# Performance work log

Measured on AMD Instinct MI355X. Metric: run time of the kernel, lower is better.

## Reference

```python
import jax, jax.numpy as jnp
import numpy as np

B, S, C = 2, 4096, 2048
H, D = 16, 128  # inner_dim = H*D = C
EPS = 1e-15     # processor self.eps
PAD_VAL = 1.0   # processor self.pad_val


def setup_inputs() -> dict:
    key = jax.random.key(0)
    ks = jax.random.split(key, 5)
    scale = C ** -0.5
    x = jax.random.normal(ks[0], (B, S, C), jnp.float32)
    Wq = jax.random.normal(ks[1], (C, C), jnp.float32) * scale
    Wk = jax.random.normal(ks[2], (C, C), jnp.float32) * scale
    Wv = jax.random.normal(ks[3], (C, C), jnp.float32) * scale
    Wo = jax.random.normal(ks[4], (C, C), jnp.float32) * scale
    bq = jnp.zeros((C,), jnp.float32)
    bk = jnp.zeros((C,), jnp.float32)
    bv = jnp.zeros((C,), jnp.float32)
    bo = jnp.zeros((C,), jnp.float32)
    # RoPE tables: pairs are adjacent (x.reshape(..., -1, 2)), so each freq repeats twice
    inv_freq = 1.0 / (10000.0 ** (np.arange(0, D, 2, dtype=np.float32) / D))
    freqs = np.outer(np.arange(S, dtype=np.float32), inv_freq)  # [S, D/2]
    emb = np.repeat(freqs, 2, axis=1)                            # [S, D]
    cos = jnp.asarray(np.cos(emb), jnp.float32)
    sin = jnp.asarray(np.sin(emb), jnp.float32)
    return {"x": x, "cos": cos, "sin": sin, "Wq": Wq, "bq": bq, "Wk": Wk,
            "bk": bk, "Wv": Wv, "bv": bv, "Wo": Wo, "bo": bo}


def _rope(t, cos, sin):
    # t: [B, H, S, D]; cos/sin: [S, D]; adjacent-pair rotation
    tr = t[..., 0::2]
    ti = t[..., 1::2]
    t_rot = jnp.stack([-ti, tr], axis=-1).reshape(t.shape)
    return t * cos + t_rot * sin


def reference(x, cos, sin, Wq, bq, Wk, bk, Wv, bv, Wo, bo):
    # projections -> [B, H, S, D] (matches transpose(-1,-2).reshape(B,H,D,S) split)
    q = (x @ Wq.T + bq).reshape(B, S, H, D).transpose(0, 2, 1, 3)
    k = (x @ Wk.T + bk).reshape(B, S, H, D).transpose(0, 2, 1, 3)
    v = (x @ Wv.T + bv).reshape(B, S, H, D).transpose(0, 2, 1, 3)
    # RoPE on q and k (self-attention), then ReLU feature map
    q = jax.nn.relu(_rope(q, cos, sin))
    k = jax.nn.relu(_rope(k, cos, sin))
    # pad value with ones along head_dim: torch F.pad(value,(0,0,0,1),value=1.0)
    v_pad = jnp.concatenate([v, jnp.full((B, H, S, 1), PAD_VAL, v.dtype)], axis=-1)  # [B,H,S,D+1]
    # linear attention: vk = value @ key  -> [B,H,D+1,D];  hs = vk @ query -> [B,H,D+1,S]
    vk = jnp.einsum('bhsn,bhsd->bhnd', v_pad, k)
    hs = jnp.einsum('bhnd,bhsd->bhns', vk, q)
    # eps-normalize by the padded-ones channel
    hs = hs[:, :, :-1] / (hs[:, :, -1:] + EPS)  # [B,H,D,S]
    out = hs.transpose(0, 3, 1, 2).reshape(B, S, H * D)  # view(B,H*D,S).permute(0,2,1)
    return out @ Wo.T + bo
```

## Files before the change

### kernel.cpp

```cpp
#include <hip/hip_runtime.h>


typedef unsigned short u16;
typedef __attribute__((ext_vector_type(8))) short bf16x8;
typedef __attribute__((ext_vector_type(4))) float f32x4;

__device__ __forceinline__ float bf2f(u16 u) {
    union { unsigned int i; float f; } x; x.i = ((unsigned int)u) << 16; return x.f;
}
__device__ __forceinline__ u16 f2bf(float f) {
    union { unsigned int i; float f; } x; x.f = f;
    unsigned int i = x.i;
    return (u16)((i + 0x7fffu + ((i >> 16) & 1u)) >> 16);
}
__device__ __forceinline__ uint4 pack8(const float* __restrict__ src) {
    float4 f0 = *(const float4*)(src);
    float4 f1 = *(const float4*)(src + 4);
    union { u16 u[8]; uint4 v; } P;
    P.u[0] = f2bf(f0.x); P.u[1] = f2bf(f0.y); P.u[2] = f2bf(f0.z); P.u[3] = f2bf(f0.w);
    P.u[4] = f2bf(f1.x); P.u[5] = f2bf(f1.y); P.u[6] = f2bf(f1.z); P.u[7] = f2bf(f1.w);
    return P.v;
}
__device__ __forceinline__ void gll16(void* lds, const void* g) {
    __builtin_amdgcn_global_load_lds(
        (const __attribute__((address_space(1))) unsigned int*)g,
        (__attribute__((address_space(3))) unsigned int*)lds, 16, 0, 0);
}

__global__ __launch_bounds__(256) void cast_all(
    const float* __restrict__ x,  const float* __restrict__ Wq,
    const float* __restrict__ Wk, const float* __restrict__ Wv,
    const float* __restrict__ Wo,
    u16* __restrict__ Xb, u16* __restrict__ Wqkvb, u16* __restrict__ Wob)
{
    int bid = blockIdx.x, t = threadIdx.x;
    const float* s; u16* d; size_t i;
    if (bid < 8192)       { s = x;  d = Xb;              i = (size_t)bid * 256 + t; }
    else if (bid < 10240) { s = Wq; d = Wqkvb;           i = (size_t)(bid - 8192)  * 256 + t; }
    else if (bid < 12288) { s = Wk; d = Wqkvb + 4194304; i = (size_t)(bid - 10240) * 256 + t; }
    else if (bid < 14336) { s = Wv; d = Wqkvb + 8388608; i = (size_t)(bid - 12288) * 256 + t; }
    else                  { s = Wo; d = Wob;             i = (size_t)(bid - 14336) * 256 + t; }
    *(uint4*)(d + i * 8) = pack8(s + i * 8);
}

__global__ __launch_bounds__(256) void gemm_qkv(
    const u16* __restrict__ Xb, const u16* __restrict__ Wqkvb,
    const float* __restrict__ bq, const float* __restrict__ bk, const float* __restrict__ bv,
    const float* __restrict__ cosT, const float* __restrict__ sinT,
    u16* __restrict__ Q, u16* __restrict__ K, u16* __restrict__ V)
{
    __shared__ __align__(16) u16 As[2 * 128 * 32];
    __shared__ __align__(16) u16 Bs[2 * 128 * 32];

    int t  = threadIdx.x;
    int bm = blockIdx.x;
    int bn = blockIdx.y;
    int region = bn >> 4;
    const u16*   W    = Wqkvb + (size_t)region * 4194304;
    const float* bias = (region == 0) ? bq : (region == 1 ? bk : bv);
    u16* OUT          = (region == 0) ? Q  : (region == 1 ? K  : V);

    int m0 = bm * 128;
    int n0 = (bn & 15) * 128;

    int w = t >> 6, lane = t & 63, quad = lane >> 4, l16 = lane & 15;
    int wm0 = (w >> 1) * 64, wn0 = (w & 1) * 64;
    int w32 = w * 32;
    int lr  = lane >> 2;
    int lc  = (lane & 3) * 8;

    const u16* ga = Xb + (size_t)(m0 + w32 + lr) * 2048 + lc;
    const u16* gb = W  + (size_t)(n0 + w32 + lr) * 2048 + lc;

    f32x4 acc[4][4] = {};

    for (int k0 = 0; k0 < 2048; k0 += 64) {
        __syncthreads();
#pragma unroll
        for (int p = 0; p < 2; p++) {
            gll16(As + p * 4096 + (size_t)w32 * 32,        ga + k0 + p * 32);
            gll16(As + p * 4096 + (size_t)(w32 + 16) * 32, ga + k0 + p * 32 + 16 * 2048);
            gll16(Bs + p * 4096 + (size_t)w32 * 32,        gb + k0 + p * 32);
            gll16(Bs + p * 4096 + (size_t)(w32 + 16) * 32, gb + k0 + p * 32 + 16 * 2048);
        }
        __syncthreads();

#pragma unroll
        for (int kk = 0; kk < 2; kk++) {
            bf16x8 af[4], bfr[4];
#pragma unroll
            for (int i = 0; i < 4; i++) af[i]  = *(const bf16x8*)(As + kk * 4096 + (wm0 + i * 16 + l16) * 32 + quad * 8);
#pragma unroll
            for (int j = 0; j < 4; j++) bfr[j] = *(const bf16x8*)(Bs + kk * 4096 + (wn0 + j * 16 + l16) * 32 + quad * 8);
#pragma unroll
            for (int i = 0; i < 4; i++)
#pragma unroll
                for (int j = 0; j < 4; j++)
                    acc[i][j] = __builtin_amdgcn_mfma_f32_16x16x32_bf16(af[i], bfr[j], acc[i][j], 0, 0, 0);
        }
    }

#pragma unroll
    for (int i = 0; i < 4; i++) {
#pragma unroll
        for (int j = 0; j < 4; j++) {
            int nc   = n0 + wn0 + j * 16 + l16;
            int h    = nc >> 7, dpos = nc & 127;
            float bia = bias[nc];
#pragma unroll
            for (int r = 0; r < 4; r++) {
                int mr = m0 + wm0 + i * 16 + quad * 4 + r;
                int b  = mr >> 12, s = mr & 4095;
                float val = acc[i][j][r] + bia;
                if (region < 2) {
                    float pair = __shfl_xor(val, 1, 64);
                    float c  = cosT[s * 128 + dpos];
                    float sn = sinT[s * 128 + dpos];
                    val = fmaxf(val * c + ((dpos & 1) ? pair : -pair) * sn, 0.f);
                }
                OUT[((size_t)(b * 16 + h) * 4096 + s) * 128 + dpos] = f2bf(val);
            }
        }
    }
}

__global__ __launch_bounds__(256) void ksum_kernel(
    const u16* __restrict__ Kb, float* __restrict__ ksumbuf)
{
    int bh = blockIdx.x, sc8 = blockIdx.y, t = threadIdx.x;
    int dpair = (t & 63) * 2, sq = t >> 6;
    const u16* base = Kb + (size_t)bh * 524288 + (size_t)(sc8 * 512 + sq * 128) * 128 + dpair;
    float s0 = 0.f, s1 = 0.f;
#pragma unroll 8
    for (int r = 0; r < 128; r++) {
        unsigned int wv = *(const unsigned int*)(base + (size_t)r * 128);
        s0 += bf2f((u16)(wv & 0xffff));
        s1 += bf2f((u16)(wv >> 16));
    }
    __shared__ float red[4][128];
    red[sq][dpair]     = s0;
    red[sq][dpair + 1] = s1;
    __syncthreads();
    if (t < 128) {
        float tot = red[0][t] + red[1][t] + red[2][t] + red[3][t];
        atomicAdd(&ksumbuf[bh * 128 + t], tot);
    }
}

__device__ __forceinline__ int vkswz(int r, int s) {
    return r * 32 + (((( s >> 3) + (r >> 3)) & 3) << 3) + (s & 7);
}

__global__ __launch_bounds__(256) void vk_mfma(
    const u16* __restrict__ Kb, const u16* __restrict__ Vb, float* __restrict__ part)
{
    int bh = blockIdx.x;
    int sk = blockIdx.y;
    int t  = threadIdx.x;
    int s0 = sk * 512;

    __shared__ __align__(16) u16 Kt[128 * 32];
    __shared__ __align__(16) u16 Vt[128 * 32];

    const u16* Kp = Kb + (size_t)bh * 524288;
    const u16* Vp = Vb + (size_t)bh * 524288;

    int dgrp  = t & 15;
    int d0    = dgrp * 8;
    int spair = (t >> 4) * 2;
    int sg    = spair >> 3;

    int w = t >> 6, lane = t & 63, quad = lane >> 4, l16 = lane & 15;
    int nbase = (w >> 1) * 64, dbase = (w & 1) * 64;

    f32x4 acc[4][4] = {};

    for (int tile = 0; tile < 16; tile++) {
        int st = s0 + tile * 32;
        __syncthreads();
        {
            const u16* kg = Kp + (size_t)(st + spair) * 128 + d0;
            const u16* vg = Vp + (size_t)(st + spair) * 128 + d0;
            union { uint4 v; u16 u[8]; } ka, kb, va, vb;
            ka.v = *(const uint4*)kg;  kb.v = *(const uint4*)(kg + 128);
            va.v = *(const uint4*)vg;  vb.v = *(const uint4*)(vg + 128);
            int swz = (((sg + dgrp) & 3) << 3) + (spair & 7);
#pragma unroll
            for (int i = 0; i < 8; i++) {
                int e = (d0 + i) * 32 + swz;
                *(unsigned int*)(Kt + e) = (unsigned int)ka.u[i] | ((unsigned int)kb.u[i] << 16);
                *(unsigned int*)(Vt + e) = (unsigned int)va.u[i] | ((unsigned int)vb.u[i] << 16);
            }
        }
        __syncthreads();

        bf16x8 af[4], bfr[4];
#pragma unroll
        for (int i = 0; i < 4; i++) {
            int r = nbase + i * 16 + l16;
            af[i] = *(const bf16x8*)(Vt + r * 32 + (((quad + (r >> 3)) & 3) << 3));
        }
#pragma unroll
        for (int j = 0; j < 4; j++) {
            int r = dbase + j * 16 + l16;
            bfr[j] = *(const bf16x8*)(Kt + r * 32 + (((quad + (r >> 3)) & 3) << 3));
        }
#pragma unroll
        for (int i = 0; i < 4; i++)
#pragma unroll
            for (int j = 0; j < 4; j++)
                acc[i][j] = __builtin_amdgcn_mfma_f32_16x16x32_bf16(af[i], bfr[j], acc[i][j], 0, 0, 0);
    }

    float* dst = part + (size_t)(bh * 8 + sk) * 16384;
#pragma unroll
    for (int i = 0; i < 4; i++) {
#pragma unroll
        for (int j = 0; j < 4; j++) {
#pragma unroll
            for (int r = 0; r < 4; r++) {
                int n = nbase + i * 16 + quad * 4 + r;
                int d = dbase + j * 16 + l16;
                dst[n * 128 + d] = acc[i][j][r];
            }
        }
    }
}

__global__ __launch_bounds__(256) void vk_reduce(const float* __restrict__ part,
                                                 float* __restrict__ vkf)
{
    int bh = blockIdx.x, by = blockIdx.y, t = threadIdx.x;
    int end = (by + 1) * 2048;
    for (int idx = by * 2048 + t; idx < end; idx += 256) {
        float s = 0.f;
#pragma unroll
        for (int p = 0; p < 8; p++) s += part[(size_t)(bh * 8 + p) * 16384 + idx];
        vkf[(size_t)bh * 16384 + idx] = s;
    }
}

__global__ __launch_bounds__(256) void hs_mfma(
    const u16* __restrict__ Qb, const float* __restrict__ vkf,
    const float* __restrict__ ksumbuf, u16* __restrict__ HS)
{
    int bh = blockIdx.x, sc = blockIdx.y;
    __shared__ __align__(16) u16 qL[128 * 136];
    __shared__ __align__(16) u16 vkL[128 * 136];
    __shared__ float rdL[128];
    __shared__ float ksumL[128];
    int t = threadIdx.x;

    const u16*   Qp   = Qb + ((size_t)bh * 4096 + sc * 128) * 128;
    const float* vsrc = vkf + (size_t)bh * 16384;
    int row = t >> 4, colc = (t & 15) * 8;
#pragma unroll
    for (int r8 = 0; r8 < 8; r8++) {
        int rr = row + r8 * 16;
        *(uint4*)(qL  + rr * 136 + colc) = *(const uint4*)(Qp + (size_t)rr * 128 + colc);
        *(uint4*)(vkL + rr * 136 + colc) = pack8(vsrc + (size_t)rr * 128 + colc);
    }
    if (t < 128) ksumL[t] = ksumbuf[bh * 128 + t];
    __syncthreads();

    {
        int srow = t >> 1, half = t & 1;
        const u16*   q  = qL + srow * 136 + half * 64;
        const float* kp = ksumL + half * 64;
        float p = 0.f;
#pragma unroll 8
        for (int d = 0; d < 64; d += 4) {
            ushort4 qv = *(const ushort4*)(q + d);
            p += bf2f(qv.x) * kp[d] + bf2f(qv.y) * kp[d + 1]
               + bf2f(qv.z) * kp[d + 2] + bf2f(qv.w) * kp[d + 3];
        }
        p += __shfl_xor(p, 1, 64);
        if (half == 0) rdL[srow] = 1.0f / (p + 1e-15f);
    }

    int w = t >> 6, lane = t & 63, quad = lane >> 4, l16 = lane & 15;
    int wm0 = (w >> 1) * 64, wn0 = (w & 1) * 64;
    f32x4 acc[4][4] = {};
#pragma unroll
    for (int ks = 0; ks < 4; ks++) {
        bf16x8 af[4], bfr[4];
#pragma unroll
        for (int i = 0; i < 4; i++) af[i]  = *(const bf16x8*)(qL  + (wm0 + i * 16 + l16) * 136 + ks * 32 + quad * 8);
#pragma unroll
        for (int j = 0; j < 4; j++) bfr[j] = *(const bf16x8*)(vkL + (wn0 + j * 16 + l16) * 136 + ks * 32 + quad * 8);
#pragma unroll
        for (int i = 0; i < 4; i++)
#pragma unroll
            for (int j = 0; j < 4; j++)
                acc[i][j] = __builtin_amdgcn_mfma_f32_16x16x32_bf16(af[i], bfr[j], acc[i][j], 0, 0, 0);
    }
    __syncthreads();

    int b = bh >> 4, h = bh & 15;
#pragma unroll
    for (int i = 0; i < 4; i++) {
#pragma unroll
        for (int j = 0; j < 4; j++) {
#pragma unroll
            for (int r = 0; r < 4; r++) {
                int sl = wm0 + i * 16 + quad * 4 + r;
                int n  = wn0 + j * 16 + l16;
                size_t srow = (size_t)b * 4096 + sc * 128 + sl;
                HS[srow * 2048 + h * 128 + n] = f2bf(acc[i][j][r] * rdL[sl]);
            }
        }
    }
}

__global__ __launch_bounds__(256) void gemm_out(
    const u16* __restrict__ HSm, const u16* __restrict__ Wob,
    const float* __restrict__ bo, float* __restrict__ OUT)
{
    __shared__ __align__(16) u16 As[2 * 128 * 32];
    __shared__ __align__(16) u16 Bs[2 * 128 * 32];

    int t  = threadIdx.x;
    int m0 = blockIdx.x * 128;
    int n0 = blockIdx.y * 128;

    int w = t >> 6, lane = t & 63, quad = lane >> 4, l16 = lane & 15;
    int wm0 = (w >> 1) * 64, wn0 = (w & 1) * 64;
    int w32 = w * 32;
    int lr  = lane >> 2;
    int lc  = (lane & 3) * 8;

    const u16* ga = HSm + (size_t)(m0 + w32 + lr) * 2048 + lc;
    const u16* gb = Wob + (size_t)(n0 + w32 + lr) * 2048 + lc;

    f32x4 acc[4][4] = {};

    for (int k0 = 0; k0 < 2048; k0 += 64) {
        __syncthreads();
#pragma unroll
        for (int p = 0; p < 2; p++) {
            gll16(As + p * 4096 + (size_t)w32 * 32,        ga + k0 + p * 32);
            gll16(As + p * 4096 + (size_t)(w32 + 16) * 32, ga + k0 + p * 32 + 16 * 2048);
            gll16(Bs + p * 4096 + (size_t)w32 * 32,        gb + k0 + p * 32);
            gll16(Bs + p * 4096 + (size_t)(w32 + 16) * 32, gb + k0 + p * 32 + 16 * 2048);
        }
        __syncthreads();

#pragma unroll
        for (int kk = 0; kk < 2; kk++) {
            bf16x8 af[4], bfr[4];
#pragma unroll
            for (int i = 0; i < 4; i++) af[i]  = *(const bf16x8*)(As + kk * 4096 + (wm0 + i * 16 + l16) * 32 + quad * 8);
#pragma unroll
            for (int j = 0; j < 4; j++) bfr[j] = *(const bf16x8*)(Bs + kk * 4096 + (wn0 + j * 16 + l16) * 32 + quad * 8);
#pragma unroll
            for (int i = 0; i < 4; i++)
#pragma unroll
                for (int j = 0; j < 4; j++)
                    acc[i][j] = __builtin_amdgcn_mfma_f32_16x16x32_bf16(af[i], bfr[j], acc[i][j], 0, 0, 0);
        }
    }

#pragma unroll
    for (int i = 0; i < 4; i++) {
#pragma unroll
        for (int j = 0; j < 4; j++) {
            int nc = n0 + wn0 + j * 16 + l16;
            float bia = bo[nc];
#pragma unroll
            for (int r = 0; r < 4; r++) {
                int mr = m0 + wm0 + i * 16 + quad * 4 + r;
                OUT[(size_t)mr * 2048 + nc] = acc[i][j][r] + bia;
            }
        }
    }
}

extern "C" void kernel_launch(void* const* d_in, const int* in_sizes, int n_in,
                              void* d_out, int out_size, void* d_ws, size_t ws_size,
                              hipStream_t stream) {
    const float* x    = (const float*)d_in[0];
    const float* cosT = (const float*)d_in[1];
    const float* sinT = (const float*)d_in[2];
    const float* Wq   = (const float*)d_in[3];
    const float* bq   = (const float*)d_in[4];
    const float* Wk   = (const float*)d_in[5];
    const float* bk   = (const float*)d_in[6];
    const float* Wv   = (const float*)d_in[7];
    const float* bv   = (const float*)d_in[8];
    const float* Wo   = (const float*)d_in[9];
    const float* bo   = (const float*)d_in[10];

    char* ws = (char*)d_ws;
    u16*   Wqkvb   = (u16*)(ws);
    u16*   Wob     = (u16*)(ws + 25165824);
    u16*   Xb      = (u16*)(ws + 33554432);
    float* part    = (float*)(ws + 33554432);
    u16*   V       = (u16*)(ws + 67108864);
    u16*   HS      = V;
    float* vkf     = (float*)(ws + 100663296);
    float* ksumbuf = (float*)(ws + 102760448);

    u16* Q  = (u16*)d_out;
    u16* Kb = (u16*)d_out + 16777216;

    hipMemsetAsync(ksumbuf, 0, 32 * 128 * sizeof(float), stream);
    cast_all<<<16384, 256, 0, stream>>>(x, Wq, Wk, Wv, Wo, Xb, Wqkvb, Wob);
    gemm_qkv<<<dim3(64, 48), 256, 0, stream>>>(Xb, Wqkvb, bq, bk, bv, cosT, sinT, Q, Kb, V);
    ksum_kernel<<<dim3(32, 8), 256, 0, stream>>>(Kb, ksumbuf);
    vk_mfma<<<dim3(32, 8), 256, 0, stream>>>(Kb, V, part);
    vk_reduce<<<dim3(32, 8), 256, 0, stream>>>(part, vkf);
    hs_mfma<<<dim3(32, 32), 256, 0, stream>>>(Q, vkf, ksumbuf, HS);
    gemm_out<<<dim3(64, 16), 256, 0, stream>>>(HS, Wob, bo, (float*)d_out);
}
```

Measured before the change: 587.3 us.

## Shrink GEMM K-step to 32 and store reduced vk as bf16

The QKV and output GEMMs now stage a single 32-wide K slice per iteration instead of two, halving LDS use per block but doubling the number of barrier pairs per tile. Separately, vk_reduce writes the reduced vk matrix as bf16, so hs_mfma loads it directly into LDS without re-packing from fp32 in every block. The GEMM change trades fewer LDS bytes (possibly higher occupancy) for more synchronisation and less latency hiding per K step. The vk change removes redundant conversion work.

```diff
diff --git a/kernel.cpp b/kernel.cpp
--- a/kernel.cpp
+++ b/kernel.cpp
@@ -49,8 +49,8 @@
     const float* __restrict__ cosT, const float* __restrict__ sinT,
     u16* __restrict__ Q, u16* __restrict__ K, u16* __restrict__ V)
 {
-    __shared__ __align__(16) u16 As[2 * 128 * 32];
-    __shared__ __align__(16) u16 Bs[2 * 128 * 32];
+    __shared__ __align__(16) u16 As[128 * 32];
+    __shared__ __align__(16) u16 Bs[128 * 32];
 
     int t  = threadIdx.x;
     int bm = blockIdx.x;
@@ -74,30 +74,24 @@
 
     f32x4 acc[4][4] = {};
 
-    for (int k0 = 0; k0 < 2048; k0 += 64) {
-        __syncthreads();
-#pragma unroll
-        for (int p = 0; p < 2; p++) {
-            gll16(As + p * 4096 + (size_t)w32 * 32,        ga + k0 + p * 32);
-            gll16(As + p * 4096 + (size_t)(w32 + 16) * 32, ga + k0 + p * 32 + 16 * 2048);
-            gll16(Bs + p * 4096 + (size_t)w32 * 32,        gb + k0 + p * 32);
-            gll16(Bs + p * 4096 + (size_t)(w32 + 16) * 32, gb + k0 + p * 32 + 16 * 2048);
-        }
-        __syncthreads();
-
-#pragma unroll
-        for (int kk = 0; kk < 2; kk++) {
-            bf16x8 af[4], bfr[4];
-#pragma unroll
-            for (int i = 0; i < 4; i++) af[i]  = *(const bf16x8*)(As + kk * 4096 + (wm0 + i * 16 + l16) * 32 + quad * 8);
-#pragma unroll
-            for (int j = 0; j < 4; j++) bfr[j] = *(const bf16x8*)(Bs + kk * 4096 + (wn0 + j * 16 + l16) * 32 + quad * 8);
-#pragma unroll
-            for (int i = 0; i < 4; i++)
-#pragma unroll
-                for (int j = 0; j < 4; j++)
-                    acc[i][j] = __builtin_amdgcn_mfma_f32_16x16x32_bf16(af[i], bfr[j], acc[i][j], 0, 0, 0);
-        }
+    for (int k0 = 0; k0 < 2048; k0 += 32) {
+        __syncthreads();
+        gll16(As + (size_t)w32 * 32,        ga + k0);
+        gll16(As + (size_t)(w32 + 16) * 32, ga + k0 + 16 * 2048);
+        gll16(Bs + (size_t)w32 * 32,        gb + k0);
+        gll16(Bs + (size_t)(w32 + 16) * 32, gb + k0 + 16 * 2048);
+        __syncthreads();
+
+        bf16x8 af[4], bfr[4];
+#pragma unroll
+        for (int i = 0; i < 4; i++) af[i]  = *(const bf16x8*)(As + (wm0 + i * 16 + l16) * 32 + quad * 8);
+#pragma unroll
+        for (int j = 0; j < 4; j++) bfr[j] = *(const bf16x8*)(Bs + (wn0 + j * 16 + l16) * 32 + quad * 8);
+#pragma unroll
+        for (int i = 0; i < 4; i++)
+#pragma unroll
+            for (int j = 0; j < 4; j++)
+                acc[i][j] = __builtin_amdgcn_mfma_f32_16x16x32_bf16(af[i], bfr[j], acc[i][j], 0, 0, 0);
     }
 
 #pragma unroll
@@ -147,10 +141,6 @@
     }
 }
 
-__device__ __forceinline__ int vkswz(int r, int s) {
-    return r * 32 + (((( s >> 3) + (r >> 3)) & 3) << 3) + (s & 7);
-}
-
 __global__ __launch_bounds__(256) void vk_mfma(
     const u16* __restrict__ Kb, const u16* __restrict__ Vb, float* __restrict__ part)
 {
@@ -228,7 +218,7 @@
 }
 
 __global__ __launch_bounds__(256) void vk_reduce(const float* __restrict__ part,
-                                                 float* __restrict__ vkf)
+                                                 u16* __restrict__ vkb)
 {
     int bh = blockIdx.x, by = blockIdx.y, t = threadIdx.x;
     int end = (by + 1) * 2048;
@@ -236,12 +226,12 @@
         float s = 0.f;
 #pragma unroll
         for (int p = 0; p < 8; p++) s += part[(size_t)(bh * 8 + p) * 16384 + idx];
-        vkf[(size_t)bh * 16384 + idx] = s;
+        vkb[(size_t)bh * 16384 + idx] = f2bf(s);
     }
 }
 
 __global__ __launch_bounds__(256) void hs_mfma(
-    const u16* __restrict__ Qb, const float* __restrict__ vkf,
+    const u16* __restrict__ Qb, const u16* __restrict__ vkb,
     const float* __restrict__ ksumbuf, u16* __restrict__ HS)
 {
     int bh = blockIdx.x, sc = blockIdx.y;
@@ -251,14 +241,14 @@
     __shared__ float ksumL[128];
     int t = threadIdx.x;
 
-    const u16*   Qp   = Qb + ((size_t)bh * 4096 + sc * 128) * 128;
-    const float* vsrc = vkf + (size_t)bh * 16384;
+    const u16* Qp   = Qb  + ((size_t)bh * 4096 + sc * 128) * 128;
+    const u16* vsrc = vkb + (size_t)bh * 16384;
     int row = t >> 4, colc = (t & 15) * 8;
 #pragma unroll
     for (int r8 = 0; r8 < 8; r8++) {
         int rr = row + r8 * 16;
-        *(uint4*)(qL  + rr * 136 + colc) = *(const uint4*)(Qp + (size_t)rr * 128 + colc);
-        *(uint4*)(vkL + rr * 136 + colc) = pack8(vsrc + (size_t)rr * 128 + colc);
+        *(uint4*)(qL  + rr * 136 + colc) = *(const uint4*)(Qp   + (size_t)rr * 128 + colc);
+        *(uint4*)(vkL + rr * 136 + colc) = *(const uint4*)(vsrc + (size_t)rr * 128 + colc);
     }
     if (t < 128) ksumL[t] = ksumbuf[bh * 128 + t];
     __syncthreads();
@@ -316,8 +306,8 @@
     const u16* __restrict__ HSm, const u16* __restrict__ Wob,
     const float* __restrict__ bo, float* __restrict__ OUT)
 {
-    __shared__ __align__(16) u16 As[2 * 128 * 32];
-    __shared__ __align__(16) u16 Bs[2 * 128 * 32];
+    __shared__ __align__(16) u16 As[128 * 32];
+    __shared__ __align__(16) u16 Bs[128 * 32];
 
     int t  = threadIdx.x;
     int m0 = blockIdx.x * 128;
@@ -334,30 +324,24 @@
 
     f32x4 acc[4][4] = {};
 
-    for (int k0 = 0; k0 < 2048; k0 += 64) {
-        __syncthreads();
-#pragma unroll
-        for (int p = 0; p < 2; p++) {
-            gll16(As + p * 4096 + (size_t)w32 * 32,        ga + k0 + p * 32);
-            gll16(As + p * 4096 + (size_t)(w32 + 16) * 32, ga + k0 + p * 32 + 16 * 2048);
-            gll16(Bs + p * 4096 + (size_t)w32 * 32,        gb + k0 + p * 32);
-            gll16(Bs + p * 4096 + (size_t)(w32 + 16) * 32, gb + k0 + p * 32 + 16 * 2048);
-        }
-        __syncthreads();
-
-#pragma unroll
-        for (int kk = 0; kk < 2; kk++) {
-            bf16x8 af[4], bfr[4];
-#pragma unroll
-            for (int i = 0; i < 4; i++) af[i]  = *(const bf16x8*)(As + kk * 4096 + (wm0 + i * 16 + l16) * 32 + quad * 8);
-#pragma unroll
-            for (int j = 0; j < 4; j++) bfr[j] = *(const bf16x8*)(Bs + kk * 4096 + (wn0 + j * 16 + l16) * 32 + quad * 8);
-#pragma unroll
-            for (int i = 0; i < 4; i++)
-#pragma unroll
-                for (int j = 0; j < 4; j++)
-                    acc[i][j] = __builtin_amdgcn_mfma_f32_16x16x32_bf16(af[i], bfr[j], acc[i][j], 0, 0, 0);
-        }
+    for (int k0 = 0; k0 < 2048; k0 += 32) {
+        __syncthreads();
+        gll16(As + (size_t)w32 * 32,        ga + k0);
+        gll16(As + (size_t)(w32 + 16) * 32, ga + k0 + 16 * 2048);
+        gll16(Bs + (size_t)w32 * 32,        gb + k0);
+        gll16(Bs + (size_t)(w32 + 16) * 32, gb + k0 + 16 * 2048);
+        __syncthreads();
+
+        bf16x8 af[4], bfr[4];
+#pragma unroll
+        for (int i = 0; i < 4; i++) af[i]  = *(const bf16x8*)(As + (wm0 + i * 16 + l16) * 32 + quad * 8);
+#pragma unroll
+        for (int j = 0; j < 4; j++) bfr[j] = *(const bf16x8*)(Bs + (wn0 + j * 16 + l16) * 32 + quad * 8);
+#pragma unroll
+        for (int i = 0; i < 4; i++)
+#pragma unroll
+            for (int j = 0; j < 4; j++)
+                acc[i][j] = __builtin_amdgcn_mfma_f32_16x16x32_bf16(af[i], bfr[j], acc[i][j], 0, 0, 0);
     }
 
 #pragma unroll
@@ -397,8 +381,8 @@
     float* part    = (float*)(ws + 33554432);
     u16*   V       = (u16*)(ws + 67108864);
     u16*   HS      = V;
-    float* vkf     = (float*)(ws + 100663296);
-    float* ksumbuf = (float*)(ws + 102760448);
+    u16*   vkb     = (u16*)(ws + 100663296);
+    float* ksumbuf = (float*)(ws + 101711872);
 
     u16* Q  = (u16*)d_out;
     u16* Kb = (u16*)d_out + 16777216;
@@ -408,7 +392,7 @@
     gemm_qkv<<<dim3(64, 48), 256, 0, stream>>>(Xb, Wqkvb, bq, bk, bv, cosT, sinT, Q, Kb, V);
     ksum_kernel<<<dim3(32, 8), 256, 0, stream>>>(Kb, ksumbuf);
     vk_mfma<<<dim3(32, 8), 256, 0, stream>>>(Kb, V, part);
-    vk_reduce<<<dim3(32, 8), 256, 0, stream>>>(part, vkf);
-    hs_mfma<<<dim3(32, 32), 256, 0, stream>>>(Q, vkf, ksumbuf, HS);
+    vk_reduce<<<dim3(32, 8), 256, 0, stream>>>(part, vkb);
+    hs_mfma<<<dim3(32, 32), 256, 0, stream>>>(Q, vkb, ksumbuf, HS);
     gemm_out<<<dim3(64, 16), 256, 0, stream>>>(HS, Wob, bo, (float*)d_out);
 }
```

Measured after the change: 574.0 us. -2.3%, faster.
